# Kernel optimization log

Hardware: AMD Instinct MI355X
Metric: run time of the kernel (lower is better)

Reference implementation:

```python
import jax, jax.numpy as jnp
import numpy as np

B, S, H, T = 32, 512, 256, 48
START_IDX, STOP_IDX = 46, 47
NEG = -10000.0


def setup_inputs() -> dict:
    key = jax.random.key(0)
    k1, k2, k3, k4, k5 = jax.random.split(key, 5)
    lstm_features = jax.random.normal(k1, (B, S, H), dtype=jnp.float32)
    emission_w = jax.random.normal(k2, (H, T), dtype=jnp.float32) * 0.02
    emission_b = jnp.zeros((T,), dtype=jnp.float32)
    transitions = jax.random.normal(k3, (T, T), dtype=jnp.float32)
    transitions = transitions.at[:, START_IDX].set(NEG).at[STOP_IDX, :].set(NEG)
    lengths = jax.random.randint(k4, (B,), S // 2, S + 1, dtype=jnp.int32)
    tags = jax.random.randint(k5, (B, S), 0, START_IDX, dtype=jnp.int32)
    return {
        'lstm_features': lstm_features,
        'emission_w': emission_w,
        'emission_b': emission_b,
        'transitions': transitions,
        'lengths': lengths,
        'tags': tags,
    }


def _crf_scores(lstm_features, emission_w, emission_b, transitions):
    # emission: [B,S,T] at the 'to' tag; crf[b,s,i,j] = emission[b,s,j] + transitions[i,j]
    em = jnp.einsum('bsh,ht->bst', lstm_features, emission_w) + emission_b
    return em[:, :, None, :] + transitions[None, None, :, :]


def _forward_alg(crf_scores, transitions, lengths):
    # alpha[b,j] = log-sum-exp over paths ending at tag j
    alpha0 = jnp.full((B, T), NEG, dtype=crf_scores.dtype).at[:, START_IDX].set(0.0)

    def step(alpha, xs):
        crf_t, t = xs  # crf_t: [B,T,T]
        tag_var = crf_t + alpha[:, :, None]  # add score of 'from' tag
        new_alpha = jax.scipy.special.logsumexp(tag_var, axis=1)  # reduce over 'from'
        alpha = jnp.where((t < lengths)[:, None], new_alpha, alpha)
        return alpha, None

    xs = (jnp.swapaxes(crf_scores, 0, 1), jnp.arange(S, dtype=lengths.dtype))
    alpha, _ = jax.lax.scan(step, alpha0, xs)
    terminal = alpha + transitions[:, STOP_IDX][None, :]
    return jax.scipy.special.logsumexp(terminal, axis=1)  # [B]


def _gold_score(crf_scores, transitions, tags, lengths):
    # from_tags[t] = START for t=0 else tags[t-1]; to_tags[t] = tags[t]
    start_col = jnp.full((B, 1), START_IDX, dtype=tags.dtype)
    from_tags = jnp.concatenate([start_col, tags[:, :-1]], axis=1)  # [B,S]
    b_idx = jnp.arange(B)[:, None]
    s_idx = jnp.arange(S)[None, :]
    sel = crf_scores[b_idx, s_idx, from_tags, tags]  # [B,S]
    mask = (s_idx < lengths[:, None]).astype(sel.dtype)
    last_tag = jnp.take_along_axis(tags, (lengths - 1)[:, None], axis=1)[:, 0]
    return jnp.sum(sel * mask, axis=1) + transitions[last_tag, STOP_IDX]  # [B]


def reference(lstm_features, emission_w, emission_b, transitions, lengths, tags):
    crf_scores = _crf_scores(lstm_features, emission_w, emission_b, transitions)
    all_paths = _forward_alg(crf_scores, transitions, lengths)
    gold = _gold_score(crf_scores, transitions, tags, lengths)
    return all_paths - gold  # per-example NLL, shape [B]
```

## Files before the change

kernel.cpp:

```cpp
#include <hip/hip_runtime.h>
#include <math.h>

#define BB 32
#define SS 512
#define HH 256
#define TT 48
#define START_IDX 46
#define STOP_IDX 47

typedef __attribute__((ext_vector_type(8))) short short8;
typedef __attribute__((ext_vector_type(4))) float floatx4;

__device__ __forceinline__ float rfl(float x) {
    return __int_as_float(__builtin_amdgcn_readfirstlane(__float_as_int(x)));
}
__device__ __forceinline__ unsigned int bf16_rne(float x) {
    const unsigned int u = __float_as_uint(x);
    return (u + 0x7fffu + ((u >> 16) & 1u)) >> 16;
}
__device__ __forceinline__ float bf2f(unsigned short h) {
    return __uint_as_float(((unsigned int)h) << 16);
}

__global__ __launch_bounds__(256) void emission_kernel(
    const float* __restrict__ f, const float* __restrict__ w,
    const float* __restrict__ bias, const float* __restrict__ trans,
    unsigned short* __restrict__ exem, uint4* __restrict__ Ebuf)
{
    __shared__ __align__(16) char smem[50176];
    __shared__ float biaslds[TT];
    unsigned short* wb = (unsigned short*)smem;
    uint4* fragbuf = (uint4*)(smem + 25600);
    float* fl = (float*)smem;

    const int tid = threadIdx.x;

    if (blockIdx.x == 0 && tid < 64) {
        const int g = tid >> 4, cl = tid & 15;
#pragma unroll
        for (int kc = 0; kc < 2; ++kc)
#pragma unroll
            for (int nt = 0; nt < 3; ++nt) {
                unsigned int p[4];
#pragma unroll
                for (int h2 = 0; h2 < 4; ++h2) {
                    const int k = kc * 32 + g * 8 + 2 * h2;
                    const int n = nt * 16 + cl;
                    const float lo = (k     < TT) ? __expf(trans[k * TT + n])       : 0.f;
                    const float hi = (k + 1 < TT) ? __expf(trans[(k + 1) * TT + n]) : 0.f;
                    p[h2] = bf16_rne(lo) | (bf16_rne(hi) << 16);
                }
                Ebuf[(kc * 3 + nt) * 64 + tid] = make_uint4(p[0], p[1], p[2], p[3]);
            }
    }

    for (int idx = tid; idx < HH * TT; idx += 256) {
        const int r = idx / TT;
        const int c = idx - r * TT;
        wb[r * 50 + c] = (unsigned short)bf16_rne(w[idx]);
    }
    if (tid < TT) biaslds[tid] = bias[tid];
    __syncthreads();

    for (int idx = tid; idx < 24 * 64; idx += 256) {
        const int fb = idx >> 6;
        const int l  = idx & 63;
        const int kt = fb / 3;
        const int nt = fb - kt * 3;
        const int kbase = kt * 32 + (l >> 4) * 8;
        const int col   = nt * 16 + (l & 15);
        unsigned int p[4];
#pragma unroll
        for (int h2 = 0; h2 < 4; ++h2) {
            const unsigned int lo = wb[(kbase + 2 * h2)     * 50 + col];
            const unsigned int hi = wb[(kbase + 2 * h2 + 1) * 50 + col];
            p[h2] = lo | (hi << 16);
        }
        fragbuf[idx] = make_uint4(p[0], p[1], p[2], p[3]);
    }
    __syncthreads();

    const int lane = tid & 63, wv = tid >> 6, g = lane >> 4, cl = lane & 15;

    short8 Bf[24];
#pragma unroll
    for (int fb = 0; fb < 24; ++fb)
        Bf[fb] = __builtin_bit_cast(short8, fragbuf[fb * 64 + lane]);
    __syncthreads();

    const int row0 = blockIdx.x * 64;
    floatx4 acc0 = {0.f,0.f,0.f,0.f}, acc1 = {0.f,0.f,0.f,0.f}, acc2 = {0.f,0.f,0.f,0.f};

    const int lr = wv * 16 + cl;
#pragma unroll
    for (int h = 0; h < 2; ++h) {
#pragma unroll
        for (int it = 0; it < 8; ++it) {
            const int idx = tid + it * 256;
            const int r = idx >> 5, k4 = idx & 31;
            const float4 v = ((const float4*)f)[(size_t)(row0 + r) * 64 + h * 32 + k4];
            *(float4*)&fl[r * 132 + k4 * 4] = v;
        }
        __syncthreads();
#pragma unroll
        for (int kt = 0; kt < 4; ++kt) {
            const float4 v0 = *(const float4*)&fl[lr * 132 + kt * 32 + g * 8];
            const float4 v1 = *(const float4*)&fl[lr * 132 + kt * 32 + g * 8 + 4];
            const unsigned int a0 = bf16_rne(v0.x) | (bf16_rne(v0.y) << 16);
            const unsigned int a1 = bf16_rne(v0.z) | (bf16_rne(v0.w) << 16);
            const unsigned int a2 = bf16_rne(v1.x) | (bf16_rne(v1.y) << 16);
            const unsigned int a3 = bf16_rne(v1.z) | (bf16_rne(v1.w) << 16);
            const short8 Af = __builtin_bit_cast(short8, make_uint4(a0, a1, a2, a3));
            const int kg = h * 4 + kt;
            acc0 = __builtin_amdgcn_mfma_f32_16x16x32_bf16(Af, Bf[kg * 3 + 0], acc0, 0, 0, 0);
            acc1 = __builtin_amdgcn_mfma_f32_16x16x32_bf16(Af, Bf[kg * 3 + 1], acc1, 0, 0, 0);
            acc2 = __builtin_amdgcn_mfma_f32_16x16x32_bf16(Af, Bf[kg * 3 + 2], acc2, 0, 0, 0);
        }
        __syncthreads();
    }

    const int outrow0 = row0 + wv * 16 + g * 4;
    const int n = cl;
#pragma unroll
    for (int r = 0; r < 4; ++r) {
        unsigned short* e = exem + (size_t)(outrow0 + r) * TT;
        e[ 0 + n] = (unsigned short)bf16_rne(__expf(acc0[r] + biaslds[ 0 + n]));
        e[16 + n] = (unsigned short)bf16_rne(__expf(acc1[r] + biaslds[16 + n]));
        e[32 + n] = (unsigned short)bf16_rne(__expf(acc2[r] + biaslds[32 + n]));
    }
}

__global__ __launch_bounds__(192) void chunk_kernel(
    const unsigned short* __restrict__ exem,
    const uint4* __restrict__ Ebuf,
    const int*   __restrict__ lengths,
    unsigned short* __restrict__ Qs,
    float* __restrict__ Ls3)
{
    __shared__ __align__(8)  unsigned short ebuf[16 * TT];
    __shared__ __align__(16) unsigned short abuf[3][17 * 56];

    const int bc = blockIdx.x, b = bc >> 5, c = bc & 31;
    const int len = lengths[b];
    int nsteps = (len - 1) - (c << 4);
    if (nsteps <= 0) return;
    if (nsteps > 16) nsteps = 16;

    const int tid = threadIdx.x;
    const int rb = tid >> 6, l = tid & 63, g = l >> 4, cl = l & 15;

    {
        const unsigned int* src = (const unsigned int*)(exem + ((size_t)b * SS + (c << 4)) * TT);
        unsigned int* dst = (unsigned int*)ebuf;
        dst[tid] = src[tid];
        dst[tid + 192] = src[tid + 192];
    }

    uint4 Bf[2][3];
#pragma unroll
    for (int kc = 0; kc < 2; ++kc)
#pragma unroll
        for (int nt = 0; nt < 3; ++nt)
            Bf[kc][nt] = Ebuf[(kc * 3 + nt) * 64 + l];

    __syncthreads();

    floatx4 acc[3];
#pragma unroll
    for (int nt = 0; nt < 3; ++nt)
#pragma unroll
        for (int r = 0; r < 4; ++r)
            acc[nt][r] = (16 * rb + 4 * g + r == nt * 16 + cl) ? 1.f : 0.f;

    float ev[3];
#pragma unroll
    for (int nt = 0; nt < 3; ++nt) ev[nt] = bf2f(ebuf[nt * 16 + cl]);

    float Lrb = 0.f;
    unsigned short* aw = abuf[rb];

    for (int s = 0; s < nsteps; ++s) {
        float scale = 1.f;
        if (s == 8) {
            const float sig = rfl(acc[0][0]);
            Lrb = __logf(sig);
            scale = __builtin_amdgcn_rcpf(sig);
        }
        const float f0 = ev[0] * scale, f1 = ev[1] * scale, f2 = ev[2] * scale;
#pragma unroll
        for (int r = 0; r < 4; ++r) {
            const int rw = (4 * g + r) * 56;
            aw[rw +      cl] = (unsigned short)bf16_rne(acc[0][r] * f0);
            aw[rw + 16 + cl] = (unsigned short)bf16_rne(acc[1][r] * f1);
            aw[rw + 32 + cl] = (unsigned short)bf16_rne(acc[2][r] * f2);
        }
        if (s + 1 < nsteps) {
#pragma unroll
            for (int nt = 0; nt < 3; ++nt)
                ev[nt] = bf2f(ebuf[(s + 1) * TT + nt * 16 + cl]);
        }
        uint4 a0 = *(const uint4*)&aw[cl * 56 + g * 8];
        uint4 a1 = *(const uint4*)&aw[cl * 56 + 32 + g * 8];
        if (g >= 2) a1 = make_uint4(0, 0, 0, 0);
        const floatx4 z = {0.f, 0.f, 0.f, 0.f};
#pragma unroll
        for (int nt = 0; nt < 3; ++nt) {
            floatx4 d = __builtin_amdgcn_mfma_f32_16x16x32_bf16(
                __builtin_bit_cast(short8, a0), __builtin_bit_cast(short8, Bf[0][nt]), z, 0, 0, 0);
            d = __builtin_amdgcn_mfma_f32_16x16x32_bf16(
                __builtin_bit_cast(short8, a1), __builtin_bit_cast(short8, Bf[1][nt]), d, 0, 0, 0);
            acc[nt] = d;
        }
    }

    unsigned short* qb = Qs + (size_t)bc * (TT * 64);
#pragma unroll
    for (int nt = 0; nt < 3; ++nt) {
        const unsigned int lo = bf16_rne(acc[nt][0]) | (bf16_rne(acc[nt][1]) << 16);
        const unsigned int hi = bf16_rne(acc[nt][2]) | (bf16_rne(acc[nt][3]) << 16);
        *(uint2*)&qb[(nt * 16 + cl) * 64 + 16 * rb + 4 * g] = make_uint2(lo, hi);
    }
    if (l == 0) Ls3[bc * 3 + rb] = Lrb;
}

__global__ __launch_bounds__(64) void finalize_kernel(
    const unsigned short* __restrict__ exem,
    const float* __restrict__ trans,
    const int*   __restrict__ lengths,
    const int*   __restrict__ tags,
    const unsigned short* __restrict__ Qs,
    const float* __restrict__ Ls3,
    float* __restrict__ out)
{
    __shared__ float tlds[TT * TT];
    __shared__ __align__(16) unsigned short vlds[64];
    __shared__ float Lsl[96];

    const int j = threadIdx.x, b = blockIdx.x, g = j >> 4, cl = j & 15;

    for (int idx = j; idx < TT * TT; idx += 64) tlds[idx] = trans[idx];

    const int len = lengths[b];
    const int nc = (len - 1 + 15) >> 4;
    for (int i = j; i < nc * 3; i += 64) Lsl[i] = Ls3[b * 96 + i];
    __builtin_amdgcn_wave_barrier();

    float gold = 0.f;
    for (int s = j; s < len; s += 64) {
        const int tag  = tags[b * SS + s];
        const int from = (s == 0) ? START_IDX : tags[b * SS + s - 1];
        gold += __logf(bf2f(exem[((size_t)b * SS + s) * TT + tag])) + tlds[from * TT + tag];
    }
    gold += __shfl_xor(gold, 32); gold += __shfl_xor(gold, 16); gold += __shfl_xor(gold, 8);
    gold += __shfl_xor(gold, 4);  gold += __shfl_xor(gold, 2);  gold += __shfl_xor(gold, 1);

    const float R0 = Lsl[0];
    float vj = 0.f;
    if (j < TT) vj = __expf(tlds[START_IDX * TT + j]) * __expf(Lsl[j >> 4] - R0);
    vlds[j] = (unsigned short)bf16_rne(vj);
    float L = R0;

    const unsigned short* qbase = Qs + (size_t)(b * 32) * (TT * 64);
    floatx4 accn[3];
    float inv = 1.f;

    uint4 pB0[3], pB1[3];
#pragma unroll
    for (int nt = 0; nt < 3; ++nt) {
        pB0[nt] = *(const uint4*)&qbase[(nt * 16 + cl) * 64 + g * 8];
        pB1[nt] = *(const uint4*)&qbase[(nt * 16 + cl) * 64 + 32 + g * 8];
    }

    for (int cc = 0; cc < nc; ++cc) {
        uint4 B0[3], B1[3];
#pragma unroll
        for (int nt = 0; nt < 3; ++nt) { B0[nt] = pB0[nt]; B1[nt] = pB1[nt]; }

        const int cn = (cc + 1 < nc) ? cc + 1 : cc;
#pragma unroll
        for (int nt = 0; nt < 3; ++nt) {
            pB0[nt] = *(const uint4*)&qbase[(size_t)cn * TT * 64 + (nt * 16 + cl) * 64 + g * 8];
            pB1[nt] = *(const uint4*)&qbase[(size_t)cn * TT * 64 + (nt * 16 + cl) * 64 + 32 + g * 8];
        }
#pragma unroll
        for (int nt = 0; nt < 3; ++nt)
            if (g >= 2) B1[nt] = make_uint4(0, 0, 0, 0);

        const uint4 A0 = *(const uint4*)&vlds[g * 8];
        const uint4 A1 = *(const uint4*)&vlds[32 + g * 8];

        const floatx4 z = {0.f, 0.f, 0.f, 0.f};
#pragma unroll
        for (int nt = 0; nt < 3; ++nt) {
            floatx4 d = __builtin_amdgcn_mfma_f32_16x16x32_bf16(
                __builtin_bit_cast(short8, A0), __builtin_bit_cast(short8, B0[nt]), z, 0, 0, 0);
            d = __builtin_amdgcn_mfma_f32_16x16x32_bf16(
                __builtin_bit_cast(short8, A1), __builtin_bit_cast(short8, B1[nt]), d, 0, 0, 0);
            accn[nt] = d;
        }

        const float sig = rfl(accn[0][0]);
        inv = __builtin_amdgcn_rcpf(sig);

        if (cc + 1 < nc) {
            const float Rn = Lsl[(cc + 1) * 3];
            const float fa0 = __expf(Lsl[(cc + 1) * 3 + 0] - Rn);
            const float fa1 = __expf(Lsl[(cc + 1) * 3 + 1] - Rn);
            const float fa2 = __expf(Lsl[(cc + 1) * 3 + 2] - Rn);
            L += __logf(sig) + Rn;
            if (j < 16) {
                vlds[ 0 + j] = (unsigned short)bf16_rne(accn[0][0] * inv * fa0);
                vlds[16 + j] = (unsigned short)bf16_rne(accn[1][0] * inv * fa1);
                vlds[32 + j] = (unsigned short)bf16_rne(accn[2][0] * inv * fa2);
            }
        } else {
            L += __logf(sig);
        }
    }

    float term = 0.f;
    if (j < 16) {
        const size_t erow = ((size_t)b * SS + (len - 1)) * TT;
#pragma unroll
        for (int nt = 0; nt < 3; ++nt) {
            const int col = nt * 16 + j;
            term += accn[nt][0] * inv * bf2f(exem[erow + col])
                    * __expf(tlds[col * TT + STOP_IDX]);
        }
    }
    term += __shfl_xor(term, 32); term += __shfl_xor(term, 16); term += __shfl_xor(term, 8);
    term += __shfl_xor(term, 4);  term += __shfl_xor(term, 2);  term += __shfl_xor(term, 1);

    if (j == 0) {
        const float all_paths = __logf(term) + L;
        const int last = tags[b * SS + len - 1];
        out[b] = all_paths - (gold + tlds[last * TT + STOP_IDX]);
    }
}

extern "C" void kernel_launch(void* const* d_in, const int* in_sizes, int n_in,
                              void* d_out, int out_size, void* d_ws, size_t ws_size,
                              hipStream_t stream) {
    const float* f       = (const float*)d_in[0];
    const float* w       = (const float*)d_in[1];
    const float* bias    = (const float*)d_in[2];
    const float* trans   = (const float*)d_in[3];
    const int*   lengths = (const int*)d_in[4];
    const int*   tags    = (const int*)d_in[5];
    float*       out     = (float*)d_out;

    char* ws = (char*)d_ws;
    unsigned short* exem = (unsigned short*)ws;
    unsigned short* Qs   = (unsigned short*)(ws + 1572864);
    float*          Lsc  = (float*)(ws + 7864320);
    uint4*          Ebuf = (uint4*)(ws + 7876608);

    emission_kernel<<<(BB * SS) / 64, 256, 0, stream>>>(f, w, bias, trans, exem, Ebuf);
    chunk_kernel<<<BB * 32, 192, 0, stream>>>(exem, Ebuf, lengths, Qs, Lsc);
    finalize_kernel<<<BB, 64, 0, stream>>>(exem, trans, lengths, tags, Qs, Lsc, out);
}
```

Measured before the change: 116.3 us.

## Parallelize finalize chunk chain across four waves via matrix-product tree

```diff
diff --git a/kernel.cpp b/kernel.cpp
--- a/kernel.cpp
+++ b/kernel.cpp
@@ -223,7 +223,7 @@
     if (l == 0) Ls3[bc * 3 + rb] = Lrb;
 }
 
-__global__ __launch_bounds__(64) void finalize_kernel(
+__global__ __launch_bounds__(256) void finalize_kernel(
     const unsigned short* __restrict__ exem,
     const float* __restrict__ trans,
     const int*   __restrict__ lengths,
@@ -233,108 +233,183 @@
     float* __restrict__ out)
 {
     __shared__ float tlds[TT * TT];
+    __shared__ __align__(16) unsigned short Mlds[4][TT * 72];
+    __shared__ __align__(16) unsigned short aw4[4][TT * 56 + 16];
+    __shared__ float Lsl[96], fal[96];
+    __shared__ float Lw[4], golds[4];
     __shared__ __align__(16) unsigned short vlds[64];
-    __shared__ float Lsl[96];
-
-    const int j = threadIdx.x, b = blockIdx.x, g = j >> 4, cl = j & 15;
-
-    for (int idx = j; idx < TT * TT; idx += 64) tlds[idx] = trans[idx];
+
+    const int tid = threadIdx.x, b = blockIdx.x;
+    const int wv = tid >> 6, l = tid & 63, g = l >> 4, cl = l & 15;
+
+    for (int idx = tid; idx < TT * TT; idx += 256) tlds[idx] = trans[idx];
 
     const int len = lengths[b];
     const int nc = (len - 1 + 15) >> 4;
-    for (int i = j; i < nc * 3; i += 64) Lsl[i] = Ls3[b * 96 + i];
-    __builtin_amdgcn_wave_barrier();
+
+    if (tid < 96) Lsl[tid] = (tid < nc * 3) ? Ls3[b * 96 + tid] : 0.f;
+    __syncthreads();
+
+    if (tid < 96) fal[tid] = __expf(Lsl[tid] - Lsl[(tid / 3) * 3]);
 
     float gold = 0.f;
-    for (int s = j; s < len; s += 64) {
+    for (int s = tid; s < len; s += 256) {
         const int tag  = tags[b * SS + s];
         const int from = (s == 0) ? START_IDX : tags[b * SS + s - 1];
         gold += __logf(bf2f(exem[((size_t)b * SS + s) * TT + tag])) + tlds[from * TT + tag];
     }
     gold += __shfl_xor(gold, 32); gold += __shfl_xor(gold, 16); gold += __shfl_xor(gold, 8);
     gold += __shfl_xor(gold, 4);  gold += __shfl_xor(gold, 2);  gold += __shfl_xor(gold, 1);
-
-    const float R0 = Lsl[0];
-    float vj = 0.f;
-    if (j < TT) vj = __expf(tlds[START_IDX * TT + j]) * __expf(Lsl[j >> 4] - R0);
-    vlds[j] = (unsigned short)bf16_rne(vj);
-    float L = R0;
-
+    if (l == 0) golds[wv] = gold;
+    __syncthreads();
+
+    const int K  = (nc + 3) >> 2;
+    const int c0 = wv * K;
+    const int c1 = (c0 + K < nc) ? (c0 + K) : nc;
+
+    floatx4 M[3][3];
+#pragma unroll
+    for (int mt = 0; mt < 3; ++mt)
+#pragma unroll
+        for (int nt = 0; nt < 3; ++nt)
+#pragma unroll
+            for (int r = 0; r < 4; ++r)
+                M[mt][nt][r] = (16 * mt + 4 * g + r == 16 * nt + cl) ? 1.f : 0.f;
+
+    float inv = 1.f, Lacc = 0.f;
+    unsigned short* aw = aw4[wv];
     const unsigned short* qbase = Qs + (size_t)(b * 32) * (TT * 64);
-    floatx4 accn[3];
-    float inv = 1.f;
 
     uint4 pB0[3], pB1[3];
-#pragma unroll
-    for (int nt = 0; nt < 3; ++nt) {
-        pB0[nt] = *(const uint4*)&qbase[(nt * 16 + cl) * 64 + g * 8];
-        pB1[nt] = *(const uint4*)&qbase[(nt * 16 + cl) * 64 + 32 + g * 8];
-    }
-
-    for (int cc = 0; cc < nc; ++cc) {
+    if (c0 < c1) {
+#pragma unroll
+        for (int nt = 0; nt < 3; ++nt) {
+            pB0[nt] = *(const uint4*)&qbase[(size_t)c0 * TT * 64 + (nt * 16 + cl) * 64 + g * 8];
+            pB1[nt] = *(const uint4*)&qbase[(size_t)c0 * TT * 64 + (nt * 16 + cl) * 64 + 32 + g * 8];
+        }
+    }
+
+    for (int c = c0; c < c1; ++c) {
         uint4 B0[3], B1[3];
 #pragma unroll
-        for (int nt = 0; nt < 3; ++nt) { B0[nt] = pB0[nt]; B1[nt] = pB1[nt]; }
-
-        const int cn = (cc + 1 < nc) ? cc + 1 : cc;
+        for (int nt = 0; nt < 3; ++nt) {
+            B0[nt] = pB0[nt];
+            B1[nt] = pB1[nt];
+            if (g >= 2) B1[nt] = make_uint4(0, 0, 0, 0);
+        }
+        const int cn = (c + 1 < c1) ? c + 1 : c;
 #pragma unroll
         for (int nt = 0; nt < 3; ++nt) {
             pB0[nt] = *(const uint4*)&qbase[(size_t)cn * TT * 64 + (nt * 16 + cl) * 64 + g * 8];
             pB1[nt] = *(const uint4*)&qbase[(size_t)cn * TT * 64 + (nt * 16 + cl) * 64 + 32 + g * 8];
         }
-#pragma unroll
-        for (int nt = 0; nt < 3; ++nt)
-            if (g >= 2) B1[nt] = make_uint4(0, 0, 0, 0);
-
-        const uint4 A0 = *(const uint4*)&vlds[g * 8];
-        const uint4 A1 = *(const uint4*)&vlds[32 + g * 8];
+
+        const float f0 = inv * fal[c * 3 + 0];
+        const float f1 = inv * fal[c * 3 + 1];
+        const float f2 = inv * fal[c * 3 + 2];
+        Lacc += Lsl[c * 3];
+
+#pragma unroll
+        for (int mt = 0; mt < 3; ++mt)
+#pragma unroll
+            for (int r = 0; r < 4; ++r) {
+                const int rw = (16 * mt + 4 * g + r) * 56;
+                aw[rw +      cl] = (unsigned short)bf16_rne(M[mt][0][r] * f0);
+                aw[rw + 16 + cl] = (unsigned short)bf16_rne(M[mt][1][r] * f1);
+                aw[rw + 32 + cl] = (unsigned short)bf16_rne(M[mt][2][r] * f2);
+            }
+
+        uint4 A0[3], A1[3];
+#pragma unroll
+        for (int mt = 0; mt < 3; ++mt) {
+            A0[mt] = *(const uint4*)&aw[(16 * mt + cl) * 56 + g * 8];
+            A1[mt] = *(const uint4*)&aw[(16 * mt + cl) * 56 + 32 + g * 8];
+            if (g >= 2) A1[mt] = make_uint4(0, 0, 0, 0);
+        }
 
         const floatx4 z = {0.f, 0.f, 0.f, 0.f};
 #pragma unroll
+        for (int mt = 0; mt < 3; ++mt)
+#pragma unroll
+            for (int nt = 0; nt < 3; ++nt) {
+                floatx4 d = __builtin_amdgcn_mfma_f32_16x16x32_bf16(
+                    __builtin_bit_cast(short8, A0[mt]), __builtin_bit_cast(short8, B0[nt]), z, 0, 0, 0);
+                d = __builtin_amdgcn_mfma_f32_16x16x32_bf16(
+                    __builtin_bit_cast(short8, A1[mt]), __builtin_bit_cast(short8, B1[nt]), d, 0, 0, 0);
+                M[mt][nt] = d;
+            }
+        const float sig = rfl(M[0][0][0]);
+        inv = __builtin_amdgcn_rcpf(sig);
+        Lacc += __logf(sig);
+    }
+
+#pragma unroll
+    for (int mt = 0; mt < 3; ++mt)
+#pragma unroll
         for (int nt = 0; nt < 3; ++nt) {
-            floatx4 d = __builtin_amdgcn_mfma_f32_16x16x32_bf16(
-                __builtin_bit_cast(short8, A0), __builtin_bit_cast(short8, B0[nt]), z, 0, 0, 0);
-            d = __builtin_amdgcn_mfma_f32_16x16x32_bf16(
-                __builtin_bit_cast(short8, A1), __builtin_bit_cast(short8, B1[nt]), d, 0, 0, 0);
-            accn[nt] = d;
-        }
-
-        const float sig = rfl(accn[0][0]);
-        inv = __builtin_amdgcn_rcpf(sig);
-
-        if (cc + 1 < nc) {
-            const float Rn = Lsl[(cc + 1) * 3];
-            const float fa0 = __expf(Lsl[(cc + 1) * 3 + 0] - Rn);
-            const float fa1 = __expf(Lsl[(cc + 1) * 3 + 1] - Rn);
-            const float fa2 = __expf(Lsl[(cc + 1) * 3 + 2] - Rn);
-            L += __logf(sig) + Rn;
-            if (j < 16) {
-                vlds[ 0 + j] = (unsigned short)bf16_rne(accn[0][0] * inv * fa0);
-                vlds[16 + j] = (unsigned short)bf16_rne(accn[1][0] * inv * fa1);
-                vlds[32 + j] = (unsigned short)bf16_rne(accn[2][0] * inv * fa2);
-            }
-        } else {
-            L += __logf(sig);
-        }
-    }
-
-    float term = 0.f;
-    if (j < 16) {
-        const size_t erow = ((size_t)b * SS + (len - 1)) * TT;
-#pragma unroll
-        for (int nt = 0; nt < 3; ++nt) {
-            const int col = nt * 16 + j;
-            term += accn[nt][0] * inv * bf2f(exem[erow + col])
-                    * __expf(tlds[col * TT + STOP_IDX]);
-        }
-    }
-    term += __shfl_xor(term, 32); term += __shfl_xor(term, 16); term += __shfl_xor(term, 8);
-    term += __shfl_xor(term, 4);  term += __shfl_xor(term, 2);  term += __shfl_xor(term, 1);
-
-    if (j == 0) {
-        const float all_paths = __logf(term) + L;
-        const int last = tags[b * SS + len - 1];
-        out[b] = all_paths - (gold + tlds[last * TT + STOP_IDX]);
+            const unsigned int lo = bf16_rne(M[mt][nt][0] * inv) | (bf16_rne(M[mt][nt][1] * inv) << 16);
+            const unsigned int hi = bf16_rne(M[mt][nt][2] * inv) | (bf16_rne(M[mt][nt][3] * inv) << 16);
+            *(uint2*)&Mlds[wv][(nt * 16 + cl) * 72 + 16 * mt + 4 * g] = make_uint2(lo, hi);
+        }
+    if (l == 0) Lw[wv] = Lacc;
+    __syncthreads();
+
+    if (wv == 0) {
+        const float vj = (l < TT) ? __expf(tlds[START_IDX * TT + l]) : 0.f;
+        vlds[l] = (unsigned short)bf16_rne(vj);
+
+        float L = 0.f, cinv = 1.f;
+        floatx4 accn[3];
+
+        for (int w = 0; w < 4; ++w) {
+            uint4 B0[3], B1[3];
+#pragma unroll
+            for (int nt = 0; nt < 3; ++nt) {
+                B0[nt] = *(const uint4*)&Mlds[w][(nt * 16 + cl) * 72 + g * 8];
+                B1[nt] = *(const uint4*)&Mlds[w][(nt * 16 + cl) * 72 + 32 + g * 8];
+                if (g >= 2) B1[nt] = make_uint4(0, 0, 0, 0);
+            }
+            const uint4 A0 = *(const uint4*)&vlds[g * 8];
+            const uint4 A1 = *(const uint4*)&vlds[32 + g * 8];
+
+            const floatx4 z = {0.f, 0.f, 0.f, 0.f};
+#pragma unroll
+            for (int nt = 0; nt < 3; ++nt) {
+                floatx4 d = __builtin_amdgcn_mfma_f32_16x16x32_bf16(
+                    __builtin_bit_cast(short8, A0), __builtin_bit_cast(short8, B0[nt]), z, 0, 0, 0);
+                d = __builtin_amdgcn_mfma_f32_16x16x32_bf16(
+                    __builtin_bit_cast(short8, A1), __builtin_bit_cast(short8, B1[nt]), d, 0, 0, 0);
+                accn[nt] = d;
+            }
+            const float sig = rfl(accn[0][0]);
+            cinv = __builtin_amdgcn_rcpf(sig);
+            L += __logf(sig) + Lw[w];
+            if (w < 3 && l < 16) {
+                vlds[ 0 + l] = (unsigned short)bf16_rne(accn[0][0] * cinv);
+                vlds[16 + l] = (unsigned short)bf16_rne(accn[1][0] * cinv);
+                vlds[32 + l] = (unsigned short)bf16_rne(accn[2][0] * cinv);
+            }
+        }
+
+        float term = 0.f;
+        if (l < 16) {
+            const size_t erow = ((size_t)b * SS + (len - 1)) * TT;
+#pragma unroll
+            for (int nt = 0; nt < 3; ++nt) {
+                const int col = nt * 16 + l;
+                term += accn[nt][0] * cinv * bf2f(exem[erow + col])
+                        * __expf(tlds[col * TT + STOP_IDX]);
+            }
+        }
+        term += __shfl_xor(term, 32); term += __shfl_xor(term, 16); term += __shfl_xor(term, 8);
+        term += __shfl_xor(term, 4);  term += __shfl_xor(term, 2);  term += __shfl_xor(term, 1);
+
+        if (l == 0) {
+            const float all_paths = __logf(term) + L;
+            const int last = tags[b * SS + len - 1];
+            out[b] = all_paths
+                     - (golds[0] + golds[1] + golds[2] + golds[3] + tlds[last * TT + STOP_IDX]);
+        }
     }
 }
 
@@ -357,5 +432,5 @@
 
     emission_kernel<<<(BB * SS) / 64, 256, 0, stream>>>(f, w, bias, trans, exem, Ebuf);
     chunk_kernel<<<BB * 32, 192, 0, stream>>>(exem, Ebuf, lengths, Qs, Lsc);
-    finalize_kernel<<<BB, 64, 0, stream>>>(exem, trans, lengths, tags, Qs, Lsc, out);
-}
+    finalize_kernel<<<BB, 256, 0, stream>>>(exem, trans, lengths, tags, Qs, Lsc, out);
+}
```

Result: faster. 109.5 us (-5.9%).
